# Performance work log

Hardware: AMD Instinct MI355X
Metric: run time of the kernel (lower is better)

## Reference

```python
import jax, jax.numpy as jnp
import numpy as np

NEG_INF = -1e38

def wkv(w, u, k, v):
    """Numerically-stable RWKV-4 WKV recurrence.
    w, u: [C] (log-space decay / first-token bonus)
    k, v: [B, T, C]
    returns y: [B, T, C]
    """
    B, T, C = k.shape

    def step(carry, kv):
        p, q, o = carry          # numerator state, denominator state, running log-max; each [B, C]
        kt, vt = kv              # [B, C]
        # output at t (includes the u-boosted current token)
        no = jnp.maximum(o, u + kt)
        A = jnp.exp(o - no)
        Bt = jnp.exp(u + kt - no)
        y = (A * p + Bt * vt) / (A * q + Bt)
        # state update (decay by w, absorb current token)
        no2 = jnp.maximum(w + o, kt)
        A2 = jnp.exp(w + o - no2)
        B2 = jnp.exp(kt - no2)
        return (A2 * p + B2 * vt, A2 * q + B2, no2), y

    init = (jnp.zeros((B, C), k.dtype), jnp.zeros((B, C), k.dtype),
            jnp.full((B, C), NEG_INF, k.dtype))
    kT = jnp.swapaxes(k, 0, 1)   # [T, B, C]
    vT = jnp.swapaxes(v, 0, 1)
    _, ys = jax.lax.scan(step, init, (kT, vT))
    return jnp.swapaxes(ys, 0, 1)


def setup_inputs() -> dict:
    key = jax.random.key(0)
    ks = jax.random.split(key, 10)
    B, T, C = 8, 4096, 512
    scale = 1.0 / np.sqrt(C)
    return {
        "x": jax.random.normal(ks[0], (B, T, C), jnp.float32),
        "spatial_decay": jax.random.normal(ks[1], (C,), jnp.float32),
        "spatial_first": jax.random.normal(ks[2], (C,), jnp.float32),
        "mix_k": jax.random.uniform(ks[3], (1, 1, C), jnp.float32),
        "mix_v": jax.random.uniform(ks[4], (1, 1, C), jnp.float32),
        "mix_r": jax.random.uniform(ks[5], (1, 1, C), jnp.float32),
        "wk": jax.random.normal(ks[6], (C, C), jnp.float32) * scale,
        "wv": jax.random.normal(ks[7], (C, C), jnp.float32) * scale,
        "wr": jax.random.normal(ks[8], (C, C), jnp.float32) * scale,
        "wo": jax.random.normal(ks[9], (C, C), jnp.float32) * scale,
    }


def reference(x, spatial_decay, spatial_first, mix_k, mix_v, mix_r, wk, wv, wr, wo):
    B, T, C = x.shape
    # time_shift: xx[t] = x[t-1], xx[0] = 0  (ZeroPad2d((0,0,1,-1)))
    xx = jnp.pad(x, ((0, 0), (1, 0), (0, 0)))[:, :-1]
    xk = x * mix_k + xx * (1.0 - mix_k)
    xv = x * mix_v + xx * (1.0 - mix_v)
    xr = x * mix_r + xx * (1.0 - mix_r)
    k = jnp.einsum('btc,cd->btd', xk, wk)
    v = jnp.einsum('btc,cd->btd', xv, wv)
    r = jnp.einsum('btc,cd->btd', xr, wr)
    sr = jax.nn.sigmoid(r)
    y = wkv(spatial_decay / T, spatial_first / T, k, v)
    return jnp.einsum('btc,cd->btd', sr * y, wo)
```

## Files before the change

### kernel.cpp

```cpp
#include <hip/hip_runtime.h>

#define BB 8
#define TT 4096
#define CC 512
#define MM (BB * TT)
#define SS 128
#define LL 32

typedef short short8 __attribute__((ext_vector_type(8)));
typedef unsigned short ushort8 __attribute__((ext_vector_type(8)));
typedef float f32x4 __attribute__((ext_vector_type(4)));

__device__ __forceinline__ unsigned short f2bf(float f) {
    unsigned int u = __float_as_uint(f);
    u += 0x7FFFu + ((u >> 16) & 1u);
    return (unsigned short)(u >> 16);
}
__device__ __forceinline__ float bf2f(unsigned short h) {
    return __uint_as_float(((unsigned int)h) << 16);
}

__device__ __forceinline__ void gl_lds16(const void* g, void* l) {
    __builtin_amdgcn_global_load_lds(
        (__attribute__((address_space(1))) void*)(unsigned long long)g,
        (__attribute__((address_space(3))) void*)(unsigned int)(unsigned long long)l,
        16, 0, 0);
}

__device__ __forceinline__ ushort8 pack8(f32x4 a, f32x4 b) {
    ushort8 r;
    r[0] = f2bf(a.x); r[1] = f2bf(a.y); r[2] = f2bf(a.z); r[3] = f2bf(a.w);
    r[4] = f2bf(b.x); r[5] = f2bf(b.y); r[6] = f2bf(b.z); r[7] = f2bf(b.w);
    return r;
}

__global__ void transpose_w(const float* __restrict__ wk, const float* __restrict__ wv,
                            const float* __restrict__ wr, const float* __restrict__ wo,
                            unsigned short* __restrict__ wT) {
    const int which = blockIdx.y;
    const float* src = (which == 0) ? wk : (which == 1) ? wv : (which == 2) ? wr : wo;
    const int i = blockIdx.x * 256 + threadIdx.x;
    const int n = i >> 9;
    const int k = i & 511;
    wT[(size_t)which * (CC * CC) + i] = f2bf(src[(size_t)k * CC + n]);
}

__global__ __launch_bounds__(256) void mix_kvr(
    const float* __restrict__ x,
    const float* __restrict__ mixk, const float* __restrict__ mixv,
    const float* __restrict__ mixr,
    unsigned short* __restrict__ kx, unsigned short* __restrict__ vx,
    unsigned short* __restrict__ rx) {
    const int idx = blockIdx.x * 256 + threadIdx.x;
    const int row = idx >> 6;
    const int ch  = (idx & 63) * 8;
    const int t   = row & (TT - 1);
    const size_t off = (size_t)row * CC + ch;
    const float* xr = x + off;

    const f32x4 zero4 = {0.f, 0.f, 0.f, 0.f};
    const f32x4 one4  = {1.f, 1.f, 1.f, 1.f};

    f32x4 xc0 = ((const f32x4*)xr)[0];
    f32x4 xc1 = ((const f32x4*)xr)[1];
    f32x4 xp0 = zero4, xp1 = zero4;
    if (t != 0) {
        xp0 = ((const f32x4*)(xr - CC))[0];
        xp1 = ((const f32x4*)(xr - CC))[1];
    }

    f32x4 m0, m1;
    m0 = ((const f32x4*)(mixk + ch))[0];
    m1 = ((const f32x4*)(mixk + ch))[1];
    *(ushort8*)(kx + off) = pack8(xc0 * m0 + xp0 * (one4 - m0),
                                  xc1 * m1 + xp1 * (one4 - m1));
    m0 = ((const f32x4*)(mixv + ch))[0];
    m1 = ((const f32x4*)(mixv + ch))[1];
    *(ushort8*)(vx + off) = pack8(xc0 * m0 + xp0 * (one4 - m0),
                                  xc1 * m1 + xp1 * (one4 - m1));
    m0 = ((const f32x4*)(mixr + ch))[0];
    m1 = ((const f32x4*)(mixr + ch))[1];
    *(ushort8*)(rx + off) = pack8(xc0 * m0 + xp0 * (one4 - m0),
                                  xc1 * m1 + xp1 * (one4 - m1));
}

__global__ __launch_bounds__(256, 2) void gemm_kvr(
    const unsigned short* __restrict__ wT,
    unsigned short* __restrict__ kbuf, unsigned short* __restrict__ vbuf,
    unsigned short* __restrict__ srb) {
    __shared__ unsigned short As[64 * 32];
    __shared__ unsigned short Bs[512 * 32];

    const int tid = threadIdx.x;
    const int pm = blockIdx.x, which = blockIdx.y;
    unsigned short* ab = (which == 0) ? kbuf : (which == 1) ? vbuf : srb;
    const unsigned short* wTw = wT + (size_t)which * (CC * CC);

    const int ar  = tid >> 2;
    const int cgs = (tid & 3) ^ ((tid >> 2) & 3);
    const unsigned short* ag = ab + (size_t)(pm * 64 + ar) * CC + cgs * 8;
    unsigned short* al = &As[tid * 8];
    const unsigned short* bgp = wTw + (size_t)ar * CC + cgs * 8;

    const int w = tid >> 6, lane = tid & 63;
    const int q = lane >> 4, l16 = lane & 15;
    const int sw = ((q ^ (l16 & 3))) * 8;

    f32x4 acc[4][8];
#pragma unroll
    for (int i = 0; i < 4; i++)
#pragma unroll
        for (int j = 0; j < 8; j++) acc[i][j] = (f32x4){0.f, 0.f, 0.f, 0.f};

    for (int kt = 0; kt < 16; ++kt) {
        const int k0 = kt * 32;
        gl_lds16(ag + k0, al);
#pragma unroll
        for (int t = 0; t < 8; ++t)
            gl_lds16(bgp + (size_t)t * 64 * CC + k0, &Bs[(t * 256 + tid) * 8]);

        __syncthreads();

        short8 a[4], b[8];
#pragma unroll
        for (int i = 0; i < 4; i++)
            a[i] = *(const short8*)&As[(i * 16 + l16) * 32 + sw];
#pragma unroll
        for (int j = 0; j < 8; j++)
            b[j] = *(const short8*)&Bs[(w * 128 + j * 16 + l16) * 32 + sw];
#pragma unroll
        for (int i = 0; i < 4; i++)
#pragma unroll
            for (int j = 0; j < 8; j++)
                acc[i][j] = __builtin_amdgcn_mfma_f32_16x16x32_bf16(a[i], b[j], acc[i][j], 0, 0, 0);

        __syncthreads();
    }

    const bool sig = (which == 2);
    const size_t rb = (size_t)pm * 64;
#pragma unroll
    for (int i = 0; i < 4; i++)
#pragma unroll
        for (int j = 0; j < 8; j++)
#pragma unroll
            for (int ii = 0; ii < 4; ii++) {
                const int m = i * 16 + q * 4 + ii;
                const int n = w * 128 + j * 16 + l16;
                float val = acc[i][j][ii];
                if (sig) val = 1.0f / (1.0f + __expf(-val));
                ab[(rb + m) * CC + n] = f2bf(val);
            }
}

__global__ __launch_bounds__(256) void wkv_part1(
    const unsigned short* __restrict__ kb, const unsigned short* __restrict__ vb,
    const float* __restrict__ sd,
    float* __restrict__ sp_, float* __restrict__ sq_, float* __restrict__ so_) {
    const int idx = blockIdx.x * 256 + threadIdx.x;
    const int c = idx & (CC - 1);
    const int b = (idx >> 9) & (BB - 1);
    const int s = idx >> 12;
    const float w = sd[c] * (1.0f / (float)TT);
    const size_t base = ((size_t)b * TT + (size_t)s * LL) * CC + c;
    const unsigned short* kp = kb + base;
    const unsigned short* vp = vb + base;

    float p = 0.f, q = 0.f, o = -1e38f;
#pragma unroll 8
    for (int i = 0; i < LL; ++i) {
        const float kt = bf2f(kp[(size_t)i * CC]);
        const float vt = bf2f(vp[(size_t)i * CC]);
        const float no2 = fmaxf(w + o, kt);
        const float A2  = __expf(w + o - no2);
        const float B2  = __expf(kt - no2);
        p = A2 * p + B2 * vt;
        q = A2 * q + B2;
        o = no2;
    }
    sp_[idx] = p; sq_[idx] = q; so_[idx] = o;
}

__global__ __launch_bounds__(256) void wkv_part2(
    const float* __restrict__ sd,
    float* __restrict__ sp_, float* __restrict__ sq_, float* __restrict__ so_) {
    const int idx = blockIdx.x * 256 + threadIdx.x;
    const int c = idx & (CC - 1);
    const float wL = sd[c] * ((float)LL / (float)TT);

    float p = 0.f, q = 0.f, o = -1e38f;
    float lp = sp_[idx], lq = sq_[idx], lo = so_[idx];
    for (int s = 0; s < SS; ++s) {
        const int off = s * (BB * CC) + idx;
        float nlp = 0.f, nlq = 0.f, nlo = 0.f;
        if (s + 1 < SS) {
            nlp = sp_[off + BB * CC];
            nlq = sq_[off + BB * CC];
            nlo = so_[off + BB * CC];
        }
        sp_[off] = p; sq_[off] = q; so_[off] = o;
        const float no = fmaxf(o + wL, lo);
        const float A  = __expf(o + wL - no);
        const float Bc = __expf(lo - no);
        p = A * p + Bc * lp;
        q = A * q + Bc * lq;
        o = no;
        lp = nlp; lq = nlq; lo = nlo;
    }
}

__global__ __launch_bounds__(256) void wkv_part3(
    const unsigned short* __restrict__ kb, const unsigned short* __restrict__ vb,
    const unsigned short* __restrict__ srb,
    const float* __restrict__ sd, const float* __restrict__ sf,
    const float* __restrict__ sp_, const float* __restrict__ sq_,
    const float* __restrict__ so_,
    unsigned short* __restrict__ zb) {
    const int idx = blockIdx.x * 256 + threadIdx.x;
    const int c = idx & (CC - 1);
    const int b = (idx >> 9) & (BB - 1);
    const int s = idx >> 12;
    const float w = sd[c] * (1.0f / (float)TT);
    const float u = sf[c] * (1.0f / (float)TT);
    const size_t base = ((size_t)b * TT + (size_t)s * LL) * CC + c;
    const unsigned short* kp = kb + base;
    const unsigned short* vp = vb + base;
    const unsigned short* sp = srb + base;
    unsigned short* zp = zb + base;

    float p = sp_[idx], q = sq_[idx], o = so_[idx];
#pragma unroll 4
    for (int i = 0; i < LL; ++i) {
        const float kt = bf2f(kp[(size_t)i * CC]);
        const float vt = bf2f(vp[(size_t)i * CC]);
        const float sr = bf2f(sp[(size_t)i * CC]);

        const float no = fmaxf(o, u + kt);
        const float A  = __expf(o - no);
        const float Bt = __expf(u + kt - no);
        const float y  = (A * p + Bt * vt) / (A * q + Bt);
        zp[(size_t)i * CC] = f2bf(sr * y);

        const float no2 = fmaxf(w + o, kt);
        const float A2  = __expf(w + o - no2);
        const float B2  = __expf(kt - no2);
        p = A2 * p + B2 * vt;
        q = A2 * q + B2;
        o = no2;
    }
}

__global__ __launch_bounds__(256, 2) void gemm_out(
    const unsigned short* __restrict__ zb, const unsigned short* __restrict__ woT,
    float* __restrict__ out) {
    __shared__ unsigned short As[128 * 32];
    __shared__ unsigned short Bs[128 * 32];

    const int tid = threadIdx.x;
    const int pm = blockIdx.x, pn = blockIdx.y;

    const int r0 = tid >> 2;
    const int cc = (tid & 3) * 8;
    const unsigned short* ag0 = zb + (size_t)(pm * 128 + r0) * CC + cc;
    const unsigned short* ag1 = ag0 + (size_t)64 * CC;
    const unsigned short* bg0 = woT + (size_t)(pn * 128 + r0) * CC + cc;
    const unsigned short* bg1 = bg0 + (size_t)64 * CC;
    unsigned short* al0 = &As[tid * 8];
    unsigned short* al1 = &As[2048 + tid * 8];
    unsigned short* bl0 = &Bs[tid * 8];
    unsigned short* bl1 = &Bs[2048 + tid * 8];

    const int wave = tid >> 6, lane = tid & 63;
    const int wr_ = wave >> 1, wc_ = wave & 1;
    const int q = lane >> 4, l16 = lane & 15;

    f32x4 acc[4][4];
#pragma unroll
    for (int i = 0; i < 4; i++)
#pragma unroll
        for (int j = 0; j < 4; j++) acc[i][j] = (f32x4){0.f, 0.f, 0.f, 0.f};

    for (int kt = 0; kt < 16; ++kt) {
        const int k0 = kt * 32;
        gl_lds16(ag0 + k0, al0);
        gl_lds16(ag1 + k0, al1);
        gl_lds16(bg0 + k0, bl0);
        gl_lds16(bg1 + k0, bl1);

        __syncthreads();

        short8 a[4], b[4];
#pragma unroll
        for (int i = 0; i < 4; i++)
            a[i] = *(const short8*)&As[(wr_ * 64 + i * 16 + l16) * 32 + q * 8];
#pragma unroll
        for (int j = 0; j < 4; j++)
            b[j] = *(const short8*)&Bs[(wc_ * 64 + j * 16 + l16) * 32 + q * 8];
#pragma unroll
        for (int i = 0; i < 4; i++)
#pragma unroll
            for (int j = 0; j < 4; j++)
                acc[i][j] = __builtin_amdgcn_mfma_f32_16x16x32_bf16(a[i], b[j], acc[i][j], 0, 0, 0);

        __syncthreads();
    }

    const int gm0 = pm * 128 + wr_ * 64;
    const int gn0 = pn * 128 + wc_ * 64;
#pragma unroll
    for (int i = 0; i < 4; i++)
#pragma unroll
        for (int j = 0; j < 4; j++)
#pragma unroll
            for (int ii = 0; ii < 4; ii++) {
                const int m = gm0 + i * 16 + q * 4 + ii;
                const int n = gn0 + j * 16 + l16;
                out[(size_t)m * CC + n] = acc[i][j][ii];
            }
}

extern "C" void kernel_launch(void* const* d_in, const int* in_sizes, int n_in,
                              void* d_out, int out_size, void* d_ws, size_t ws_size,
                              hipStream_t stream) {
    const float* x  = (const float*)d_in[0];
    const float* sd = (const float*)d_in[1];
    const float* sf = (const float*)d_in[2];
    const float* mk = (const float*)d_in[3];
    const float* mv = (const float*)d_in[4];
    const float* mr = (const float*)d_in[5];
    const float* wk = (const float*)d_in[6];
    const float* wv = (const float*)d_in[7];
    const float* wr = (const float*)d_in[8];
    const float* wo = (const float*)d_in[9];
    float* out = (float*)d_out;

    char* ws = (char*)d_ws;
    unsigned short* wT = (unsigned short*)ws;
    unsigned short* kbuf = (unsigned short*)(ws + (size_t)4 * CC * CC * 2);
    unsigned short* vbuf = kbuf + (size_t)MM * CC;
    unsigned short* srb  = vbuf + (size_t)MM * CC;
    unsigned short* zb   = srb + (size_t)MM * CC;
    float* sp_ = (float*)(zb + (size_t)MM * CC);
    float* sq_ = sp_ + (size_t)SS * BB * CC;
    float* so_ = sq_ + (size_t)SS * BB * CC;
    unsigned short* woT = wT + (size_t)3 * CC * CC;

    transpose_w<<<dim3((CC * CC) / 256, 4), 256, 0, stream>>>(wk, wv, wr, wo, wT);

    mix_kvr<<<dim3((MM * CC / 8) / 256), 256, 0, stream>>>(
        x, mk, mv, mr, kbuf, vbuf, srb);

    gemm_kvr<<<dim3(MM / 64, 3), 256, 0, stream>>>(wT, kbuf, vbuf, srb);

    wkv_part1<<<dim3((SS * BB * CC) / 256), 256, 0, stream>>>(kbuf, vbuf, sd, sp_, sq_, so_);
    wkv_part2<<<dim3((BB * CC) / 256), 256, 0, stream>>>(sd, sp_, sq_, so_);
    wkv_part3<<<dim3((SS * BB * CC) / 256), 256, 0, stream>>>(
        kbuf, vbuf, srb, sd, sf, sp_, sq_, so_, zb);

    gemm_out<<<dim3(MM / 128, CC / 128), 256, 0, stream>>>(zb, woT, out);
}
```

Baseline: 326.6 us.

## Split fused in-place KVR GEMM into three out-of-place 128x128-tiled GEMMs

```diff
diff --git a/kernel.cpp b/kernel.cpp
--- a/kernel.cpp
+++ b/kernel.cpp
@@ -84,72 +84,76 @@
                                   xc1 * m1 + xp1 * (one4 - m1));
 }
 
-__global__ __launch_bounds__(256, 2) void gemm_kvr(
-    const unsigned short* __restrict__ wT,
-    unsigned short* __restrict__ kbuf, unsigned short* __restrict__ vbuf,
-    unsigned short* __restrict__ srb) {
-    __shared__ unsigned short As[64 * 32];
-    __shared__ unsigned short Bs[512 * 32];
+__global__ __launch_bounds__(256, 2) void gemm_one(
+    const unsigned short* __restrict__ A,
+    const unsigned short* __restrict__ Bw,
+    unsigned short* __restrict__ Cb,
+    int sig) {
+    __shared__ unsigned short As[128 * 32];
+    __shared__ unsigned short Bs[128 * 32];
 
     const int tid = threadIdx.x;
-    const int pm = blockIdx.x, which = blockIdx.y;
-    unsigned short* ab = (which == 0) ? kbuf : (which == 1) ? vbuf : srb;
-    const unsigned short* wTw = wT + (size_t)which * (CC * CC);
-
-    const int ar  = tid >> 2;
-    const int cgs = (tid & 3) ^ ((tid >> 2) & 3);
-    const unsigned short* ag = ab + (size_t)(pm * 64 + ar) * CC + cgs * 8;
-    unsigned short* al = &As[tid * 8];
-    const unsigned short* bgp = wTw + (size_t)ar * CC + cgs * 8;
-
-    const int w = tid >> 6, lane = tid & 63;
+    const int pn = blockIdx.x, pm = blockIdx.y;
+
+    const int r0 = tid >> 2;
+    const int cc = (tid & 3) * 8;
+    const unsigned short* ag0 = A + (size_t)(pm * 128 + r0) * CC + cc;
+    const unsigned short* ag1 = ag0 + (size_t)64 * CC;
+    const unsigned short* bg0 = Bw + (size_t)(pn * 128 + r0) * CC + cc;
+    const unsigned short* bg1 = bg0 + (size_t)64 * CC;
+    unsigned short* al0 = &As[tid * 8];
+    unsigned short* al1 = &As[2048 + tid * 8];
+    unsigned short* bl0 = &Bs[tid * 8];
+    unsigned short* bl1 = &Bs[2048 + tid * 8];
+
+    const int wave = tid >> 6, lane = tid & 63;
+    const int wr_ = wave >> 1, wc_ = wave & 1;
     const int q = lane >> 4, l16 = lane & 15;
-    const int sw = ((q ^ (l16 & 3))) * 8;
-
-    f32x4 acc[4][8];
+
+    f32x4 acc[4][4];
 #pragma unroll
     for (int i = 0; i < 4; i++)
 #pragma unroll
-        for (int j = 0; j < 8; j++) acc[i][j] = (f32x4){0.f, 0.f, 0.f, 0.f};
+        for (int j = 0; j < 4; j++) acc[i][j] = (f32x4){0.f, 0.f, 0.f, 0.f};
 
     for (int kt = 0; kt < 16; ++kt) {
         const int k0 = kt * 32;
-        gl_lds16(ag + k0, al);
-#pragma unroll
-        for (int t = 0; t < 8; ++t)
-            gl_lds16(bgp + (size_t)t * 64 * CC + k0, &Bs[(t * 256 + tid) * 8]);
+        gl_lds16(ag0 + k0, al0);
+        gl_lds16(ag1 + k0, al1);
+        gl_lds16(bg0 + k0, bl0);
+        gl_lds16(bg1 + k0, bl1);
 
         __syncthreads();
 
-        short8 a[4], b[8];
+        short8 a[4], b[4];
 #pragma unroll
         for (int i = 0; i < 4; i++)
-            a[i] = *(const short8*)&As[(i * 16 + l16) * 32 + sw];
-#pragma unroll
-        for (int j = 0; j < 8; j++)
-            b[j] = *(const short8*)&Bs[(w * 128 + j * 16 + l16) * 32 + sw];
+            a[i] = *(const short8*)&As[(wr_ * 64 + i * 16 + l16) * 32 + q * 8];
+#pragma unroll
+        for (int j = 0; j < 4; j++)
+            b[j] = *(const short8*)&Bs[(wc_ * 64 + j * 16 + l16) * 32 + q * 8];
 #pragma unroll
         for (int i = 0; i < 4; i++)
 #pragma unroll
-            for (int j = 0; j < 8; j++)
+            for (int j = 0; j < 4; j++)
                 acc[i][j] = __builtin_amdgcn_mfma_f32_16x16x32_bf16(a[i], b[j], acc[i][j], 0, 0, 0);
 
         __syncthreads();
     }
 
-    const bool sig = (which == 2);
-    const size_t rb = (size_t)pm * 64;
+    const int gm0 = pm * 128 + wr_ * 64;
+    const int gn0 = pn * 128 + wc_ * 64;
 #pragma unroll
     for (int i = 0; i < 4; i++)
 #pragma unroll
-        for (int j = 0; j < 8; j++)
+        for (int j = 0; j < 4; j++)
 #pragma unroll
             for (int ii = 0; ii < 4; ii++) {
-                const int m = i * 16 + q * 4 + ii;
-                const int n = w * 128 + j * 16 + l16;
+                const int m = gm0 + i * 16 + q * 4 + ii;
+                const int n = gn0 + j * 16 + l16;
                 float val = acc[i][j][ii];
                 if (sig) val = 1.0f / (1.0f + __expf(-val));
-                ab[(rb + m) * CC + n] = f2bf(val);
+                Cb[(size_t)m * CC + n] = f2bf(val);
             }
 }
 
@@ -211,11 +215,10 @@
 
 __global__ __launch_bounds__(256) void wkv_part3(
     const unsigned short* __restrict__ kb, const unsigned short* __restrict__ vb,
-    const unsigned short* __restrict__ srb,
+    unsigned short* __restrict__ srz,
     const float* __restrict__ sd, const float* __restrict__ sf,
     const float* __restrict__ sp_, const float* __restrict__ sq_,
-    const float* __restrict__ so_,
-    unsigned short* __restrict__ zb) {
+    const float* __restrict__ so_) {
     const int idx = blockIdx.x * 256 + threadIdx.x;
     const int c = idx & (CC - 1);
     const int b = (idx >> 9) & (BB - 1);
@@ -225,8 +228,7 @@
     const size_t base = ((size_t)b * TT + (size_t)s * LL) * CC + c;
     const unsigned short* kp = kb + base;
     const unsigned short* vp = vb + base;
-    const unsigned short* sp = srb + base;
-    unsigned short* zp = zb + base;
+    unsigned short* sp = srz + base;
 
     float p = sp_[idx], q = sq_[idx], o = so_[idx];
 #pragma unroll 4
@@ -239,7 +241,7 @@
         const float A  = __expf(o - no);
         const float Bt = __expf(u + kt - no);
         const float y  = (A * p + Bt * vt) / (A * q + Bt);
-        zp[(size_t)i * CC] = f2bf(sr * y);
+        sp[(size_t)i * CC] = f2bf(sr * y);
 
         const float no2 = fmaxf(w + o, kt);
         const float A2  = __expf(w + o - no2);
@@ -257,7 +259,7 @@
     __shared__ unsigned short Bs[128 * 32];
 
     const int tid = threadIdx.x;
-    const int pm = blockIdx.x, pn = blockIdx.y;
+    const int pn = blockIdx.x, pm = blockIdx.y;
 
     const int r0 = tid >> 2;
     const int cc = (tid & 3) * 8;
@@ -336,26 +338,31 @@
 
     char* ws = (char*)d_ws;
     unsigned short* wT = (unsigned short*)ws;
-    unsigned short* kbuf = (unsigned short*)(ws + (size_t)4 * CC * CC * 2);
-    unsigned short* vbuf = kbuf + (size_t)MM * CC;
-    unsigned short* srb  = vbuf + (size_t)MM * CC;
-    unsigned short* zb   = srb + (size_t)MM * CC;
-    float* sp_ = (float*)(zb + (size_t)MM * CC);
+    unsigned short* buf0 = (unsigned short*)(ws + (size_t)4 * CC * CC * 2);
+    unsigned short* buf1 = buf0 + (size_t)MM * CC;
+    unsigned short* buf2 = buf1 + (size_t)MM * CC;
+    unsigned short* buf3 = buf2 + (size_t)MM * CC;
+    float* sp_ = (float*)(buf3 + (size_t)MM * CC);
     float* sq_ = sp_ + (size_t)SS * BB * CC;
     float* so_ = sq_ + (size_t)SS * BB * CC;
+    unsigned short* wkT = wT;
+    unsigned short* wvT = wT + (size_t)1 * CC * CC;
+    unsigned short* wrT = wT + (size_t)2 * CC * CC;
     unsigned short* woT = wT + (size_t)3 * CC * CC;
 
     transpose_w<<<dim3((CC * CC) / 256, 4), 256, 0, stream>>>(wk, wv, wr, wo, wT);
 
     mix_kvr<<<dim3((MM * CC / 8) / 256), 256, 0, stream>>>(
-        x, mk, mv, mr, kbuf, vbuf, srb);
-
-    gemm_kvr<<<dim3(MM / 64, 3), 256, 0, stream>>>(wT, kbuf, vbuf, srb);
-
-    wkv_part1<<<dim3((SS * BB * CC) / 256), 256, 0, stream>>>(kbuf, vbuf, sd, sp_, sq_, so_);
+        x, mk, mv, mr, buf0, buf1, buf2);
+
+    gemm_one<<<dim3(4, MM / 128), 256, 0, stream>>>(buf2, wrT, buf3, 1);
+    gemm_one<<<dim3(4, MM / 128), 256, 0, stream>>>(buf0, wkT, buf2, 0);
+    gemm_one<<<dim3(4, MM / 128), 256, 0, stream>>>(buf1, wvT, buf0, 0);
+
+    wkv_part1<<<dim3((SS * BB * CC) / 256), 256, 0, stream>>>(buf2, buf0, sd, sp_, sq_, so_);
     wkv_part2<<<dim3((BB * CC) / 256), 256, 0, stream>>>(sd, sp_, sq_, so_);
     wkv_part3<<<dim3((SS * BB * CC) / 256), 256, 0, stream>>>(
-        kbuf, vbuf, srb, sd, sf, sp_, sq_, so_, zb);
-
-    gemm_out<<<dim3(MM / 128, CC / 128), 256, 0, stream>>>(zb, woT, out);
-}
+        buf2, buf0, buf3, sd, sf, sp_, sq_, so_);
+
+    gemm_out<<<dim3(4, MM / 128), 256, 0, stream>>>(buf3, woT, out);
+}
```

Measured after the change: 334.8 us. +2.5%, slower.
